# Optimization experiments

Measured on AMD Instinct MI355X. Metric: run time of the kernel, lower is better.

The kernel has to match this reference:

```python
import jax, jax.numpy as jnp
import numpy as np

B, C, M = 8192, 1024, 4096  # batch, controller width, memory_size


def setup_inputs() -> dict:
    key = jax.random.key(0)
    k1, k2, k3 = jax.random.split(key, 3)
    memory = jax.random.normal(k1, (B, M), dtype=jnp.float32)
    controller_output = jax.random.normal(k2, (B, C), dtype=jnp.float32)
    W = jax.random.normal(k3, (C, M), dtype=jnp.float32) * 0.02  # Dense kernel
    b = jnp.zeros((M,), dtype=jnp.float32)                       # Dense bias
    return {"memory": memory, "controller_output": controller_output, "W": W, "b": b}


def _l2_normalize(x, eps=1e-12):
    # matches tf.linalg.l2_normalize: x / sqrt(max(sum(x^2), eps))
    return x / jnp.sqrt(jnp.maximum(jnp.sum(x * x, axis=-1, keepdims=True), eps))


def reference(memory, controller_output, W, b):
    # Dense key projection followed by softmax over memory width
    key_vec = jax.nn.softmax(controller_output @ W + b, axis=-1)        # [B, M]
    # tf.keras.losses.cosine_similarity = -sum(l2n(a) * l2n(b), -1)
    sims = -jnp.sum(_l2_normalize(key_vec) * _l2_normalize(memory), axis=-1)  # [B]
    read_weights = jax.nn.softmax(sims, axis=-1)                        # softmax over B (as in source)
    read_vector = jnp.sum(read_weights[:, None] * memory, axis=1)       # [B]
    return read_vector
```

## Files before the change

kernel.cpp:

```cpp
#include <hip/hip_runtime.h>

#define NB 8192
#define NC 1024
#define NM 4096
#define NCH 16

typedef __attribute__((ext_vector_type(8))) short bf16x8;
typedef __attribute__((ext_vector_type(4))) float f32x4;

__device__ __forceinline__ unsigned short f2bf(float x) {
  unsigned int u = __float_as_uint(x);
  u += 0x7FFFu + ((u >> 16) & 1u);
  return (unsigned short)(u >> 16);
}
__device__ __forceinline__ float bf2f(unsigned short h) {
  return __uint_as_float(((unsigned int)h) << 16);
}
__device__ __forceinline__ unsigned int pk2(float a, float b) {
  return (unsigned int)f2bf(a) | ((unsigned int)f2bf(b) << 16);
}

__device__ __forceinline__ void gload_lds16(const void* g, void* l) {
  __builtin_amdgcn_global_load_lds(
      (const __attribute__((address_space(1))) unsigned int*)g,
      (__attribute__((address_space(3))) unsigned int*)l, 16, 0, 0);
}

#define DSR(dst, addr, IMM) \
  asm volatile("ds_read_b128 %0, %1 offset:" IMM : "=v"(dst) : "v"(addr))

#define BAR asm volatile("s_barrier" ::: "memory")
#define SBAR __builtin_amdgcn_sched_barrier(0)
#define LGKM0 asm volatile("s_waitcnt lgkmcnt(0)" ::: "memory")

__global__ __launch_bounds__(256) void prep_k(const float* __restrict__ W,
                                              unsigned short* __restrict__ Wt,
                                              const float* __restrict__ coin,
                                              unsigned short* __restrict__ Abf) {
  __shared__ float tile[64][65];
  const int bid = blockIdx.x;
  const int t = threadIdx.x;
  if (bid < 1024) {
    const int n0 = (bid & 63) * 64, k0 = (bid >> 6) * 64;
    const int r = t >> 2, q = t & 3;
    const float4* src = reinterpret_cast<const float4*>(W + (size_t)(k0 + r) * NM + n0 + q * 16);
    float4 x0 = src[0], x1 = src[1], x2 = src[2], x3 = src[3];
    float* tr = &tile[r][q * 16];
    tr[0]=x0.x; tr[1]=x0.y; tr[2]=x0.z;  tr[3]=x0.w;
    tr[4]=x1.x; tr[5]=x1.y; tr[6]=x1.z;  tr[7]=x1.w;
    tr[8]=x2.x; tr[9]=x2.y; tr[10]=x2.z; tr[11]=x2.w;
    tr[12]=x3.x; tr[13]=x3.y; tr[14]=x3.z; tr[15]=x3.w;
    __syncthreads();
    unsigned int pk[8];
#pragma unroll
    for (int i = 0; i < 8; ++i)
      pk[i] = pk2(tile[q * 16 + 2 * i][r], tile[q * 16 + 2 * i + 1][r]);
    int4* dst = reinterpret_cast<int4*>(Wt + (size_t)(n0 + r) * NC + k0 + q * 16);
    dst[0] = make_int4((int)pk[0], (int)pk[1], (int)pk[2], (int)pk[3]);
    dst[1] = make_int4((int)pk[4], (int)pk[5], (int)pk[6], (int)pk[7]);
  } else {
    const size_t i = ((size_t)(bid - 1024) * 256 + t) * 8;
    const float4* s = reinterpret_cast<const float4*>(coin + i);
    float4 x0 = s[0], x1 = s[1];
    int4 o = make_int4((int)pk2(x0.x, x0.y), (int)pk2(x0.z, x0.w),
                       (int)pk2(x1.x, x1.y), (int)pk2(x1.z, x1.w));
    *reinterpret_cast<int4*>(Abf + i) = o;
  }
}

__global__ __launch_bounds__(512) void gemm_fused(
    const unsigned short* __restrict__ Abf, const float* __restrict__ memry,
    const unsigned short* __restrict__ Wt, const float* __restrict__ bvec,
    float* __restrict__ pdotg, float* __restrict__ pesqg,
    float* __restrict__ pmsqg, float* __restrict__ pmsg) {
  __shared__ __align__(16) unsigned short LDS[2][4][8192];
  const int bm = blockIdx.x, bn = blockIdx.y;
  const int row0 = bm * 256, col0 = bn * 256;
  const int t = threadIdx.x;
  const int wid = t >> 6, lane = t & 63;
  const int wr = wid >> 2, wc = wid & 3;
  const int l15 = lane & 15, lg = lane >> 4;
  const int ga8 = (lg ^ ((l15 >> 1) & 3)) * 8;

  f32x4 acc[8][4];
#pragma unroll
  for (int mi = 0; mi < 8; ++mi)
#pragma unroll
    for (int ni = 0; ni < 4; ++ni) acc[mi][ni] = (f32x4){0.f, 0.f, 0.f, 0.f};

  const unsigned ldsbase =
      (unsigned)(uintptr_t)(__attribute__((address_space(3))) void*)&LDS[0][0][0];
  const unsigned abase = ldsbase + ((wr * 128 + l15) * 32 + ga8) * 2;
  const unsigned bbase = ldsbase + 32768 + ((wc * 64 + l15) * 32 + ga8) * 2;

  const int srow0 = t >> 2;
  const int sk8 = ((t & 3) ^ ((srow0 >> 1) & 3)) * 8;
  const unsigned short* gA = Abf + (size_t)(row0 + srow0) * NC + sk8;
  const unsigned short* gB = Wt + (size_t)(col0 + srow0) * NC + sk8;

#define STG(SL, TY, KT)                                                      \
  {                                                                          \
    const unsigned short* s0 = ((TY) <= 1 ? gA : gB) + (KT) * 64 + ((TY)&1) * 32; \
    gload_lds16(s0, &LDS[SL][TY][t * 8]);                                    \
    gload_lds16(s0 + (size_t)128 * NC, &LDS[SL][TY][t * 8 + 4096]);          \
  }
#define NOSTG
#define VM8 asm volatile("s_waitcnt vmcnt(8)" ::: "memory")
#define VM4 asm volatile("s_waitcnt vmcnt(4)" ::: "memory")
#define VM0 asm volatile("s_waitcnt vmcnt(0)" ::: "memory")
#define NOVM

#define MFMG0(UA, UB, MI)                                                    \
  _Pragma("unroll") for (int ni = 0; ni < 4; ++ni)                           \
      acc[MI][ni] = __builtin_amdgcn_mfma_f32_16x16x32_bf16(                 \
          UA[MI], UB[ni], acc[MI][ni], 0, 0, 0);
#define MFMG1(UA, UB, MI)                                                    \
  _Pragma("unroll") for (int ni = 0; ni < 4; ++ni)                           \
      acc[4 + (MI)][ni] = __builtin_amdgcn_mfma_f32_16x16x32_bf16(           \
          UA[MI], UB[ni], acc[4 + (MI)][ni], 0, 0, 0);

#define PH(UA, UB, VA, VB, DOREAD, NSL, NS, CSL, CS, STG1, STG2, VM)         \
  {                                                                          \
    LGKM0;                                                                   \
    SBAR;                                                                    \
    __builtin_amdgcn_s_setprio(1);                                           \
    MFMG0(UA, UB, 0);                                                        \
    SBAR;                                                                    \
    if (DOREAD) {                                                            \
      const unsigned ba = bbase + (NSL)*65536 + (NS)*16384;                  \
      DSR(VB[0], ba, "0");    DSR(VB[1], ba, "1024");                        \
      DSR(VB[2], ba, "2048"); DSR(VB[3], ba, "3072");                        \
    }                                                                        \
    SBAR;                                                                    \
    MFMG0(UA, UB, 1);                                                        \
    SBAR;                                                                    \
    if (DOREAD) {                                                            \
      const unsigned aa = abase + (NSL)*65536 + (NS)*16384;                  \
      DSR(VA[0], aa, "0");    DSR(VA[1], aa, "1024");                        \
      DSR(VA[2], aa, "2048"); DSR(VA[3], aa, "3072");                        \
    }                                                                        \
    SBAR;                                                                    \
    MFMG0(UA, UB, 2);                                                        \
    SBAR;                                                                    \
    STG1;                                                                    \
    SBAR;                                                                    \
    MFMG0(UA, UB, 3);                                                        \
    SBAR;                                                                    \
    {                                                                        \
      const unsigned ca = abase + (CSL)*65536 + (CS)*16384 + 4096;           \
      DSR(UA[0], ca, "0");    DSR(UA[1], ca, "1024");                        \
      DSR(UA[2], ca, "2048"); DSR(UA[3], ca, "3072");                        \
    }                                                                        \
    SBAR;                                                                    \
    LGKM0;                                                                   \
    SBAR;                                                                    \
    MFMG1(UA, UB, 0);                                                        \
    SBAR;                                                                    \
    STG2;                                                                    \
    SBAR;                                                                    \
    MFMG1(UA, UB, 1);                                                        \
    SBAR;                                                                    \
    VM;                                                                      \
    SBAR;                                                                    \
    MFMG1(UA, UB, 2);                                                        \
    MFMG1(UA, UB, 3);                                                        \
    __builtin_amdgcn_s_setprio(0);                                           \
    BAR;                                                                     \
    SBAR;                                                                    \
  }

  STG(0, 0, 0); STG(0, 2, 0); STG(0, 1, 0); STG(0, 3, 0);
  STG(1, 0, 1); STG(1, 2, 1); STG(1, 1, 1); STG(1, 3, 1);
  VM8;
  BAR;
  SBAR;

  bf16x8 xA[4], xB[4], yA[4], yB[4];
  {
    DSR(xB[0], bbase, "0");    DSR(xB[1], bbase, "1024");
    DSR(xB[2], bbase, "2048"); DSR(xB[3], bbase, "3072");
    DSR(xA[0], abase, "0");    DSR(xA[1], abase, "1024");
    DSR(xA[2], abase, "2048"); DSR(xA[3], abase, "3072");
  }

  PH(xA, xB, yA, yB, 1, 0, 1, 0, 0, NOSTG, NOSTG, VM4);
  for (int it = 0; it < 7; ++it) {
    const int c2 = 2 * it + 2, c3 = 2 * it + 3;
    PH(yA, yB, xA, xB, 1, 1, 0, 0, 1, STG(0, 0, c2), STG(0, 2, c2), VM4);
    PH(xA, xB, yA, yB, 1, 1, 1, 1, 0, STG(0, 1, c2), STG(0, 3, c2), VM4);
    PH(yA, yB, xA, xB, 1, 0, 0, 1, 1, STG(1, 0, c3), STG(1, 2, c3), VM4);
    PH(xA, xB, yA, yB, 1, 0, 1, 0, 0, STG(1, 1, c3), STG(1, 3, c3), VM4);
  }
  PH(yA, yB, xA, xB, 1, 1, 0, 0, 1, NOSTG, NOSTG, VM0);
  PH(xA, xB, yA, yB, 1, 1, 1, 1, 0, NOSTG, NOSTG, NOVM);
  PH(yA, yB, xA, xB, 0, 0, 0, 1, 1, NOSTG, NOSTG, NOVM);
#undef PH
#undef MFMG0
#undef MFMG1
#undef STG

  LGKM0;
  unsigned short (*e_lds)[256] = reinterpret_cast<unsigned short(*)[256]>(&LDS[0][0][0]);
  float bv[4];
#pragma unroll
  for (int ni = 0; ni < 4; ++ni) bv[ni] = bvec[col0 + wc * 64 + ni * 16 + l15];
#pragma unroll
  for (int mi = 0; mi < 8; ++mi)
#pragma unroll
    for (int ni = 0; ni < 4; ++ni)
#pragma unroll
      for (int j = 0; j < 4; ++j) {
        const int rl = wr * 128 + mi * 16 + 4 * lg + j;
        const int cl = wc * 64 + ni * 16 + l15;
        e_lds[rl][cl ^ (((rl >> 2) & 3) << 4)] = f2bf(__expf(acc[mi][ni][j] + bv[ni]));
      }
  __syncthreads();

  {
    const int halfl = lane >> 5, l31 = lane & 31;
    const int rbase = wid * 32;
#pragma unroll 8
    for (int i = 0; i < 16; ++i) {
      const int rl = rbase + 2 * i + halfl;
      const float4* mp = reinterpret_cast<const float4*>(
          memry + (size_t)(row0 + rl) * NM + col0 + l31 * 8);
      float4 m0 = mp[0], m1 = mp[1];
      bf16x8 ev = *reinterpret_cast<const bf16x8*>(
          &e_lds[rl][(l31 * 8) ^ (((rl >> 2) & 3) << 4)]);
      float mv[8] = {m0.x, m0.y, m0.z, m0.w, m1.x, m1.y, m1.z, m1.w};
      float pd = 0.f, pe = 0.f, pq = 0.f, pm = 0.f;
#pragma unroll
      for (int k = 0; k < 8; ++k) {
        float e = bf2f((unsigned short)ev[k]);
        pd += e * mv[k]; pe += e * e; pq += mv[k] * mv[k]; pm += mv[k];
      }
#pragma unroll
      for (int sh = 1; sh < 32; sh <<= 1) {
        pd += __shfl_xor(pd, sh); pe += __shfl_xor(pe, sh);
        pq += __shfl_xor(pq, sh); pm += __shfl_xor(pm, sh);
      }
      if (l31 == 0) {
        const int idx = (row0 + rl) * NCH + bn;
        pdotg[idx] = pd; pesqg[idx] = pe; pmsqg[idx] = pq; pmsg[idx] = pm;
      }
    }
  }
}

__global__ __launch_bounds__(256) void finalize_k(
    const float* __restrict__ pd, const float* __restrict__ pe,
    const float* __restrict__ pq, const float* __restrict__ pm,
    float* __restrict__ sims, float* __restrict__ mst) {
  const int r = blockIdx.x * 256 + threadIdx.x;
  float d = 0.f, e = 0.f, q = 0.f, m = 0.f;
#pragma unroll
  for (int i = 0; i < NCH; ++i) {
    d += pd[r * NCH + i];
    e += pe[r * NCH + i];
    q += pq[r * NCH + i];
    m += pm[r * NCH + i];
  }
  sims[r] = -d / (sqrtf(fmaxf(e, 1e-12f)) * sqrtf(fmaxf(q, 1e-12f)));
  mst[r] = m;
}

__global__ __launch_bounds__(1024) void softmax_out_k(
    const float* __restrict__ sims, const float* __restrict__ mst,
    float* __restrict__ out) {
  __shared__ float red[16];
  const int t = threadIdx.x;
  float v[8];
  float mx = -1e30f;
#pragma unroll
  for (int i = 0; i < 8; ++i) {
    v[i] = sims[t + i * 1024];
    mx = fmaxf(mx, v[i]);
  }
#pragma unroll
  for (int s = 1; s < 64; s <<= 1) mx = fmaxf(mx, __shfl_xor(mx, s));
  if ((t & 63) == 0) red[t >> 6] = mx;
  __syncthreads();
  float m2 = red[0];
#pragma unroll
  for (int i = 1; i < 16; ++i) m2 = fmaxf(m2, red[i]);
  mx = m2;
  float sum = 0.f;
#pragma unroll
  for (int i = 0; i < 8; ++i) sum += __expf(v[i] - mx);
#pragma unroll
  for (int s = 1; s < 64; s <<= 1) sum += __shfl_xor(sum, s);
  __syncthreads();
  if ((t & 63) == 0) red[t >> 6] = sum;
  __syncthreads();
  float s2 = 0.f;
#pragma unroll
  for (int i = 0; i < 16; ++i) s2 += red[i];
  const float inv = 1.0f / s2;
#pragma unroll
  for (int i = 0; i < 8; ++i)
    out[t + i * 1024] = __expf(v[i] - mx) * inv * mst[t + i * 1024];
}

extern "C" void kernel_launch(void* const* d_in, const int* in_sizes, int n_in,
                              void* d_out, int out_size, void* d_ws, size_t ws_size,
                              hipStream_t stream) {
  const float* memry = (const float*)d_in[0];
  const float* co    = (const float*)d_in[1];
  const float* W     = (const float*)d_in[2];
  const float* bvec  = (const float*)d_in[3];
  float* out = (float*)d_out;

  char* w = (char*)d_ws;
  unsigned short* Wt  = (unsigned short*)w;
  unsigned short* Abf = Wt + (size_t)NM * NC;
  float* pdot = (float*)(Abf + (size_t)NB * NC);
  float* pesq = pdot + (size_t)NB * NCH;
  float* pmsq = pesq + (size_t)NB * NCH;
  float* pms  = pmsq + (size_t)NB * NCH;
  float* sims = pms  + (size_t)NB * NCH;
  float* mst  = sims + NB;

  prep_k<<<1024 + (size_t)NB * NC / (256 * 8), 256, 0, stream>>>(W, Wt, co, Abf);
  gemm_fused<<<dim3(NB / 256, NM / 256), 512, 0, stream>>>(Abf, memry, Wt, bvec,
                                                           pdot, pesq, pmsq, pms);
  finalize_k<<<NB / 256, 256, 0, stream>>>(pdot, pesq, pmsq, pms, sims, mst);
  softmax_out_k<<<1, 1024, 0, stream>>>(sims, mst, out);
}
```

Measured before the change: 103.9 us.

## Load W operand directly from global into registers, stage only A through LDS

The GEMM main loop no longer stages the W (B operand) tile through LDS. Each wave now issues global_load_dwordx4 directly into MFMA operand registers, while only the A tile goes through a 4-slot LDS ring with a reworked k-step schedule and vmcnt waits. This halves the LDS traffic and removes the ds_read for B. The cost is that each wave fetches its B fragment from global/L2 with no sharing across waves in the block, and global latency must be hidden within one phase.

```diff
diff --git a/kernel.cpp b/kernel.cpp
--- a/kernel.cpp
+++ b/kernel.cpp
@@ -73,7 +73,7 @@
     const unsigned short* __restrict__ Wt, const float* __restrict__ bvec,
     float* __restrict__ pdotg, float* __restrict__ pesqg,
     float* __restrict__ pmsqg, float* __restrict__ pmsg) {
-  __shared__ __align__(16) unsigned short LDS[2][4][8192];
+  __shared__ __align__(16) unsigned short LDS[65536];
   const int bm = blockIdx.x, bn = blockIdx.y;
   const int row0 = bm * 256, col0 = bn * 256;
   const int t = threadIdx.x;
@@ -89,26 +89,33 @@
     for (int ni = 0; ni < 4; ++ni) acc[mi][ni] = (f32x4){0.f, 0.f, 0.f, 0.f};
 
   const unsigned ldsbase =
-      (unsigned)(uintptr_t)(__attribute__((address_space(3))) void*)&LDS[0][0][0];
+      (unsigned)(uintptr_t)(__attribute__((address_space(3))) void*)&LDS[0];
   const unsigned abase = ldsbase + ((wr * 128 + l15) * 32 + ga8) * 2;
-  const unsigned bbase = ldsbase + 32768 + ((wc * 64 + l15) * 32 + ga8) * 2;
 
   const int srow0 = t >> 2;
   const int sk8 = ((t & 3) ^ ((srow0 >> 1) & 3)) * 8;
   const unsigned short* gA = Abf + (size_t)(row0 + srow0) * NC + sk8;
-  const unsigned short* gB = Wt + (size_t)(col0 + srow0) * NC + sk8;
-
-#define STG(SL, TY, KT)                                                      \
-  {                                                                          \
-    const unsigned short* s0 = ((TY) <= 1 ? gA : gB) + (KT) * 64 + ((TY)&1) * 32; \
-    gload_lds16(s0, &LDS[SL][TY][t * 8]);                                    \
-    gload_lds16(s0 + (size_t)128 * NC, &LDS[SL][TY][t * 8 + 4096]);          \
-  }
-#define NOSTG
-#define VM8 asm volatile("s_waitcnt vmcnt(8)" ::: "memory")
-#define VM4 asm volatile("s_waitcnt vmcnt(4)" ::: "memory")
+
+  unsigned voff0 = (((unsigned)(col0 + wc * 64 + 0 * 16 + l15) * NC) + lg * 8) * 2;
+  unsigned voff1 = voff0 + 16 * NC * 2;
+  unsigned voff2 = voff1 + 16 * NC * 2;
+  unsigned voff3 = voff2 + 16 * NC * 2;
+
+#define BLD4(VB)                                                                  \
+  {                                                                               \
+    asm volatile("global_load_dwordx4 %0, %1, %2" : "=v"(VB[0]) : "v"(voff0), "s"(Wt)); \
+    asm volatile("global_load_dwordx4 %0, %1, %2" : "=v"(VB[1]) : "v"(voff1), "s"(Wt)); \
+    asm volatile("global_load_dwordx4 %0, %1, %2" : "=v"(VB[2]) : "v"(voff2), "s"(Wt)); \
+    asm volatile("global_load_dwordx4 %0, %1, %2" : "=v"(VB[3]) : "v"(voff3), "s"(Wt)); \
+    voff0 += 64; voff1 += 64; voff2 += 64; voff3 += 64;                           \
+  }
+#define STGA(U, KHW)                                                   \
+  {                                                                    \
+    gload_lds16(gA + (KHW), &LDS[(U)*8192 + t * 8]);                   \
+    gload_lds16(gA + 128 * NC + (KHW), &LDS[(U)*8192 + 4096 + t * 8]); \
+  }
+#define VM2 asm volatile("s_waitcnt vmcnt(2)" ::: "memory")
 #define VM0 asm volatile("s_waitcnt vmcnt(0)" ::: "memory")
-#define NOVM
 
 #define MFMG0(UA, UB, MI)                                                    \
   _Pragma("unroll") for (int ni = 0; ni < 4; ++ni)                           \
@@ -119,35 +126,30 @@
       acc[4 + (MI)][ni] = __builtin_amdgcn_mfma_f32_16x16x32_bf16(           \
           UA[MI], UB[ni], acc[4 + (MI)][ni], 0, 0, 0);
 
-#define PH(UA, UB, VA, VB, DOREAD, NSL, NS, CSL, CS, STG1, STG2, VM)         \
+#define PH(UA, UB, VA, VB, DOB, DOVA, DOSTG, UNXT, UCUR, KHW, VM)            \
   {                                                                          \
+    VM;                                                                      \
     LGKM0;                                                                   \
     SBAR;                                                                    \
     __builtin_amdgcn_s_setprio(1);                                           \
     MFMG0(UA, UB, 0);                                                        \
     SBAR;                                                                    \
-    if (DOREAD) {                                                            \
-      const unsigned ba = bbase + (NSL)*65536 + (NS)*16384;                  \
-      DSR(VB[0], ba, "0");    DSR(VB[1], ba, "1024");                        \
-      DSR(VB[2], ba, "2048"); DSR(VB[3], ba, "3072");                        \
-    }                                                                        \
+    if (DOB) BLD4(VB);                                                       \
     SBAR;                                                                    \
     MFMG0(UA, UB, 1);                                                        \
     SBAR;                                                                    \
-    if (DOREAD) {                                                            \
-      const unsigned aa = abase + (NSL)*65536 + (NS)*16384;                  \
+    if (DOVA) {                                                              \
+      const unsigned aa = abase + (UNXT)*16384;                              \
       DSR(VA[0], aa, "0");    DSR(VA[1], aa, "1024");                        \
       DSR(VA[2], aa, "2048"); DSR(VA[3], aa, "3072");                        \
     }                                                                        \
     SBAR;                                                                    \
     MFMG0(UA, UB, 2);                                                        \
     SBAR;                                                                    \
-    STG1;                                                                    \
-    SBAR;                                                                    \
     MFMG0(UA, UB, 3);                                                        \
     SBAR;                                                                    \
     {                                                                        \
-      const unsigned ca = abase + (CSL)*65536 + (CS)*16384 + 4096;           \
+      const unsigned ca = abase + (UCUR)*16384 + 4096;                       \
       DSR(UA[0], ca, "0");    DSR(UA[1], ca, "1024");                        \
       DSR(UA[2], ca, "2048"); DSR(UA[3], ca, "3072");                        \
     }                                                                        \
@@ -156,11 +158,9 @@
     SBAR;                                                                    \
     MFMG1(UA, UB, 0);                                                        \
     SBAR;                                                                    \
-    STG2;                                                                    \
+    if (DOSTG) STGA(UCUR, KHW);                                              \
     SBAR;                                                                    \
     MFMG1(UA, UB, 1);                                                        \
-    SBAR;                                                                    \
-    VM;                                                                      \
     SBAR;                                                                    \
     MFMG1(UA, UB, 2);                                                        \
     MFMG1(UA, UB, 3);                                                        \
@@ -169,38 +169,36 @@
     SBAR;                                                                    \
   }
 
-  STG(0, 0, 0); STG(0, 2, 0); STG(0, 1, 0); STG(0, 3, 0);
-  STG(1, 0, 1); STG(1, 2, 1); STG(1, 1, 1); STG(1, 3, 1);
-  VM8;
+  bf16x8 xA[4], xB[4], yA[4], yB[4];
+
+  STGA(0, 0);
+  BLD4(xB);
+  STGA(1, 32); STGA(2, 64); STGA(3, 96);
+  VM2;
   BAR;
   SBAR;
-
-  bf16x8 xA[4], xB[4], yA[4], yB[4];
-  {
-    DSR(xB[0], bbase, "0");    DSR(xB[1], bbase, "1024");
-    DSR(xB[2], bbase, "2048"); DSR(xB[3], bbase, "3072");
-    DSR(xA[0], abase, "0");    DSR(xA[1], abase, "1024");
-    DSR(xA[2], abase, "2048"); DSR(xA[3], abase, "3072");
-  }
-
-  PH(xA, xB, yA, yB, 1, 0, 1, 0, 0, NOSTG, NOSTG, VM4);
+  DSR(xA[0], abase, "0");    DSR(xA[1], abase, "1024");
+  DSR(xA[2], abase, "2048"); DSR(xA[3], abase, "3072");
+
   for (int it = 0; it < 7; ++it) {
-    const int c2 = 2 * it + 2, c3 = 2 * it + 3;
-    PH(yA, yB, xA, xB, 1, 1, 0, 0, 1, STG(0, 0, c2), STG(0, 2, c2), VM4);
-    PH(xA, xB, yA, yB, 1, 1, 1, 1, 0, STG(0, 1, c2), STG(0, 3, c2), VM4);
-    PH(yA, yB, xA, xB, 1, 0, 0, 1, 1, STG(1, 0, c3), STG(1, 2, c3), VM4);
-    PH(xA, xB, yA, yB, 1, 0, 1, 0, 0, STG(1, 1, c3), STG(1, 3, c3), VM4);
-  }
-  PH(yA, yB, xA, xB, 1, 1, 0, 0, 1, NOSTG, NOSTG, VM0);
-  PH(xA, xB, yA, yB, 1, 1, 1, 1, 0, NOSTG, NOSTG, NOVM);
-  PH(yA, yB, xA, xB, 0, 0, 0, 1, 1, NOSTG, NOSTG, NOVM);
+    const int k0 = 32 * (4 * it + 4);
+    PH(xA, xB, yA, yB, 1, 1, 1, 1, 0, k0,      VM2);
+    PH(yA, yB, xA, xB, 1, 1, 1, 2, 1, k0 + 32, VM2);
+    PH(xA, xB, yA, yB, 1, 1, 1, 3, 2, k0 + 64, VM2);
+    PH(yA, yB, xA, xB, 1, 1, 1, 0, 3, k0 + 96, VM2);
+  }
+  PH(xA, xB, yA, yB, 1, 1, 0, 1, 0, 0, VM2);
+  PH(yA, yB, xA, xB, 1, 1, 0, 2, 1, 0, VM0);
+  PH(xA, xB, yA, yB, 1, 1, 0, 3, 2, 0, VM0);
+  PH(yA, yB, xA, xB, 0, 0, 0, 0, 3, 0, VM0);
 #undef PH
 #undef MFMG0
 #undef MFMG1
-#undef STG
+#undef STGA
+#undef BLD4
 
   LGKM0;
-  unsigned short (*e_lds)[256] = reinterpret_cast<unsigned short(*)[256]>(&LDS[0][0][0]);
+  unsigned short (*e_lds)[256] = reinterpret_cast<unsigned short(*)[256]>(&LDS[0]);
   float bv[4];
 #pragma unroll
   for (int ni = 0; ni < 4; ++ni) bv[ni] = bvec[col0 + wc * 64 + ni * 16 + l15];
```

Measured after the change: 122.9 us. +18.2%, slower.
